# Optimization experiments

Measured on AMD Instinct MI355X. Metric: run time of the kernel, lower is better.

## Reference

```python
import jax, jax.numpy as jnp
import numpy as np

EXPR_NUM = 80
N_PTS = 2_000_000


def setup_inputs() -> dict:
    key = jax.random.key(0)
    ks = jax.random.split(key, 16)
    L, C = 64, 32
    return {
        "expr": jax.random.normal(ks[0], (EXPR_NUM,), jnp.float32) * 0.1,
        "jaw_quat_weight": jax.random.normal(ks[1], (16, 1), jnp.float32) * 0.1,
        "xyz": jax.random.uniform(ks[2], (N_PTS, 3), jnp.float32),
        "feat_lines_x": jax.random.normal(ks[3], (96, L, C), jnp.float32) * 0.02,
        "feat_lines_y": jax.random.normal(ks[4], (96, L, C), jnp.float32) * 0.02,
        "feat_lines_z": jax.random.normal(ks[5], (96, L, C), jnp.float32) * 0.02,
        "w0_v": jax.random.normal(ks[6], (128, 192), jnp.float32) * (1.0 / np.sqrt(192)),
        "w0_g": jax.random.uniform(ks[7], (128,), jnp.float32, 0.5, 1.5),
        "b0": jax.random.normal(ks[8], (128,), jnp.float32) * 0.01,
        "w1_v": jax.random.normal(ks[9], (128, 128), jnp.float32) * (1.0 / np.sqrt(128)),
        "w1_g": jax.random.uniform(ks[10], (128,), jnp.float32, 0.5, 1.5),
        "b1": jax.random.normal(ks[11], (128,), jnp.float32) * 0.01,
        "w2_v": jax.random.normal(ks[12], (1, 128), jnp.float32) * (1.0 / np.sqrt(128)),
        "w2_g": jax.random.uniform(ks[13], (1,), jnp.float32, 0.5, 1.5),
        "b2": jax.random.normal(ks[14], (1,), jnp.float32) * 0.01,
    }


def _wn_linear(x, v, g, b):
    # weight_norm: W = g * v / ||v||_row (norm over input dim)
    norm = jnp.sqrt(jnp.sum(v * v, axis=1))
    W = v * (g / norm)[:, None]
    return x @ W.T + b


def _sample_line(bs_line, jaw_line, pts):
    # bs_line, jaw_line: [L, C]; pts: [N] in [0,1]
    L = bs_line.shape[0]
    p = jnp.clip(pts, 0.0, 1.0) * (L - 1)
    li = jnp.floor(p).astype(jnp.int32)
    ri = jnp.minimum(li + 1, L - 1)
    w = (p - li.astype(p.dtype))[:, None]
    bs = bs_line[li] + w * (bs_line[ri] - bs_line[li])
    jaw = jaw_line[li] + w * (jaw_line[ri] - jaw_line[li])
    return bs, jaw


def reference(expr, jaw_quat_weight, xyz,
              feat_lines_x, feat_lines_y, feat_lines_z,
              w0_v, w0_g, b0, w1_v, w1_g, b1, w2_v, w2_g, b2):
    e = expr.reshape(-1)[:EXPR_NUM]             # [80]
    jw = jaw_quat_weight.reshape(-1)            # [16] (k=1 broadcast in torch einsum)
    # weighted sums over blendshape / jaw pose lines -> [L, C]
    bs_x = jnp.einsum('ilc,i->lc', feat_lines_x[:EXPR_NUM], e)
    bs_y = jnp.einsum('ilc,i->lc', feat_lines_y[:EXPR_NUM], e)
    bs_z = jnp.einsum('ilc,i->lc', feat_lines_z[:EXPR_NUM], e)
    jaw_x = jnp.einsum('ilc,i->lc', feat_lines_x[EXPR_NUM:], jw)
    jaw_y = jnp.einsum('ilc,i->lc', feat_lines_y[EXPR_NUM:], jw)
    jaw_z = jnp.einsum('ilc,i->lc', feat_lines_z[EXPR_NUM:], jw)
    bx, jx = _sample_line(bs_x, jaw_x, xyz[:, 0])
    by, jy = _sample_line(bs_y, jaw_y, xyz[:, 1])
    bz, jz = _sample_line(bs_z, jaw_z, xyz[:, 2])
    fea = jnp.concatenate((bx, by, bz, jx, jy, jz), axis=1)  # [N, 192]
    fea = jax.nn.relu(_wn_linear(fea, w0_v, w0_g, b0))
    fea = jax.nn.relu(_wn_linear(fea, w1_v, w1_g, b1))
    return _wn_linear(fea, w2_v, w2_g, b2)                   # [N, 1]
```

## Files before the change

### kernel.cpp

```cpp
#include <hip/hip_runtime.h>
#include <math.h>

typedef _Float16 h2 __attribute__((ext_vector_type(2)));
typedef _Float16 f16x8 __attribute__((ext_vector_type(8)));
typedef float f32x4 __attribute__((ext_vector_type(4)));


__global__ void precompute_T(const float* __restrict__ expr,
                             const float* __restrict__ jqw,
                             const float* __restrict__ flx,
                             const float* __restrict__ fly,
                             const float* __restrict__ flz,
                             const float* __restrict__ w0v,
                             const float* __restrict__ w0g,
                             const float* __restrict__ b0,
                             float* __restrict__ T) {
    int a = blockIdx.x >> 6;
    int l = blockIdx.x & 63;
    const float* fl = (a == 0) ? flx : (a == 1) ? fly : flz;
    __shared__ float bs[32];
    __shared__ float jaw[32];
    int t = threadIdx.x;
    if (t < 32) {
        float s = 0.f;
        for (int i = 0; i < 80; ++i) s += expr[i] * fl[(i * 64 + l) * 32 + t];
        bs[t] = s;
    } else if (t < 64) {
        int c = t - 32;
        float s = 0.f;
        for (int i = 0; i < 16; ++i) s += jqw[i] * fl[((80 + i) * 64 + l) * 32 + c];
        jaw[c] = s;
    }
    __syncthreads();
    int j = t;
    float ns = 0.f;
    for (int c = 0; c < 192; ++c) { float v = w0v[j * 192 + c]; ns += v * v; }
    float scale = w0g[j] / sqrtf(ns);
    float acc = 0.f;
    for (int c = 0; c < 32; ++c) acc += w0v[j * 192 + a * 32 + c] * bs[c];
    for (int c = 0; c < 32; ++c) acc += w0v[j * 192 + 96 + a * 32 + c] * jaw[c];
    acc *= scale;
    if (a == 0) acc += b0[j];
    T[(a * 64 + l) * 128 + j] = acc;
}

__global__ void precompute_W(const float* __restrict__ w1v,
                             const float* __restrict__ w1g,
                             const float* __restrict__ w2v,
                             const float* __restrict__ w2g,
                             float* __restrict__ W1n,
                             float* __restrict__ w2n) {
    int j = threadIdx.x;
    float ns = 0.f;
    for (int k = 0; k < 128; ++k) { float v = w1v[j * 128 + k]; ns += v * v; }
    float s = w1g[j] / sqrtf(ns);
    for (int k = 0; k < 128; ++k) W1n[j * 128 + k] = w1v[j * 128 + k] * s;
    float n2 = 0.f;
    for (int k = 0; k < 128; ++k) { float v = w2v[k]; n2 += v * v; }
    w2n[j] = w2v[j] * (w2g[0] / sqrtf(n2));
}

#define LDS_T_H2 12288
#define LDS_B_H2 8192

__launch_bounds__(512)
__global__ void mlp_mfma(const float* __restrict__ xyz,
                         const float* __restrict__ Tg,
                         const float* __restrict__ W1g,
                         const float* __restrict__ w2ng,
                         const float* __restrict__ b1,
                         const float* __restrict__ b2p,
                         float* __restrict__ out, int npts) {
    __shared__ __align__(16) h2 tT[LDS_T_H2];
    __shared__ __align__(16) h2 tB[LDS_B_H2];
    int tid = threadIdx.x;

    for (int pi = tid; pi < LDS_T_H2; pi += 512) {
        int r = pi >> 6;
        int p = pi & 63;
        int phys = (r << 6) | (((p >> 2) ^ (r & 15)) << 2) | (p & 3);
        h2 v;
        v.x = (_Float16)Tg[2 * pi];
        v.y = (_Float16)Tg[2 * pi + 1];
        tT[phys] = v;
    }
    for (int pi = tid; pi < LDS_B_H2; pi += 512) {
        int dp = pi & 3;
        int l  = (pi >> 2) & 63;
        int nt = (pi >> 8) & 7;
        int kk = (pi >> 11) & 3;
        int n = nt * 16 + (l & 15);
        int k = kk * 32 + (l >> 4) * 8 + 2 * dp;
        h2 v;
        v.x = (_Float16)W1g[n * 128 + k];
        v.y = (_Float16)W1g[n * 128 + k + 1];
        tB[pi] = v;
    }
    __syncthreads();

    int lane = tid & 63;
    int lp = lane & 15;
    int lg = lane >> 4;
    int waveid = blockIdx.x * 8 + (tid >> 6);
    int nwaves = gridDim.x * 8;
    int ntiles = (npts + 15) >> 4;

    float b1r[8], w2r[8];
#pragma unroll
    for (int nt = 0; nt < 8; ++nt) {
        b1r[nt] = b1[nt * 16 + lp];
        w2r[nt] = w2ng[nt * 16 + lp];
    }
    float b2 = b2p[0];

#pragma unroll 1
    for (int tile = waveid; tile < ntiles; tile += nwaves) {
        int m0 = tile << 4;
        int p = m0 + lp;
        int pc = min(p, npts - 1);
        float cx = xyz[pc * 3 + 0];
        float cy = xyz[pc * 3 + 1];
        float cz = xyz[pc * 3 + 2];

        f16x8 hA[4];
#pragma unroll
        for (int kk = 0; kk < 4; ++kk)
            hA[kk] = (f16x8){0, 0, 0, 0, 0, 0, 0, 0};

#pragma unroll
        for (int a = 0; a < 3; ++a) {
            float v = (a == 0) ? cx : (a == 1) ? cy : cz;
            v = fminf(fmaxf(v, 0.f), 1.f) * 63.f;
            float fv = floorf(v);
            int li = (int)fv;
            int ri = min(li + 1, 63);
            _Float16 w = (_Float16)(v - fv);
            _Float16 wl = (_Float16)1.0f - w;
            f16x8 w8  = {w, w, w, w, w, w, w, w};
            f16x8 wl8 = {wl, wl, wl, wl, wl, wl, wl, wl};
            int rowL = (a * 64 + li) << 4;
            int rowR = (a * 64 + ri) << 4;
            int sl = li & 15;
            int sr = ri & 15;
#pragma unroll
            for (int kk = 0; kk < 4; ++kk) {
                int cidx = lg + 4 * kk;
                f16x8 vl = *reinterpret_cast<const f16x8*>(
                    &tT[(rowL + (cidx ^ sl)) << 2]);
                f16x8 vr = *reinterpret_cast<const f16x8*>(
                    &tT[(rowR + (cidx ^ sr)) << 2]);
                hA[kk] = hA[kk] + vl * wl8 + vr * w8;
            }
        }
        f16x8 z8 = (f16x8){0, 0, 0, 0, 0, 0, 0, 0};
#pragma unroll
        for (int kk = 0; kk < 4; ++kk)
            hA[kk] = __builtin_elementwise_max(hA[kk], z8);

        f32x4 acc[8];
#pragma unroll
        for (int nt = 0; nt < 8; ++nt) acc[nt] = (f32x4){0.f, 0.f, 0.f, 0.f};

#pragma unroll
        for (int kk = 0; kk < 4; ++kk) {
#pragma unroll
            for (int nt = 0; nt < 8; ++nt) {
                f16x8 b = *reinterpret_cast<const f16x8*>(
                    &tB[(((kk * 8 + nt) << 6) | lane) << 2]);
                acc[nt] = __builtin_amdgcn_mfma_f32_16x16x32_f16(
                    hA[kk], b, acc[nt], 0, 0, 0);
            }
        }

        float part0 = 0.f, part1 = 0.f, part2 = 0.f, part3 = 0.f;
#pragma unroll
        for (int nt = 0; nt < 8; ++nt) {
            part0 += w2r[nt] * fmaxf(acc[nt][0] + b1r[nt], 0.f);
            part1 += w2r[nt] * fmaxf(acc[nt][1] + b1r[nt], 0.f);
            part2 += w2r[nt] * fmaxf(acc[nt][2] + b1r[nt], 0.f);
            part3 += w2r[nt] * fmaxf(acc[nt][3] + b1r[nt], 0.f);
        }
#pragma unroll
        for (int mask = 1; mask <= 8; mask <<= 1) {
            part0 += __shfl_xor(part0, mask, 64);
            part1 += __shfl_xor(part1, mask, 64);
            part2 += __shfl_xor(part2, mask, 64);
            part3 += __shfl_xor(part3, mask, 64);
        }
        int mbase = m0 + (lg << 2);
        if (lp == 0 && mbase + 0 < npts) out[mbase + 0] = part0 + b2;
        if (lp == 1 && mbase + 1 < npts) out[mbase + 1] = part1 + b2;
        if (lp == 2 && mbase + 2 < npts) out[mbase + 2] = part2 + b2;
        if (lp == 3 && mbase + 3 < npts) out[mbase + 3] = part3 + b2;
    }
}

extern "C" void kernel_launch(void* const* d_in, const int* in_sizes, int n_in,
                              void* d_out, int out_size, void* d_ws, size_t ws_size,
                              hipStream_t stream) {
    const float* expr = (const float*)d_in[0];
    const float* jqw  = (const float*)d_in[1];
    const float* xyz  = (const float*)d_in[2];
    const float* flx  = (const float*)d_in[3];
    const float* fly  = (const float*)d_in[4];
    const float* flz  = (const float*)d_in[5];
    const float* w0v  = (const float*)d_in[6];
    const float* w0g  = (const float*)d_in[7];
    const float* b0   = (const float*)d_in[8];
    const float* w1v  = (const float*)d_in[9];
    const float* w1g  = (const float*)d_in[10];
    const float* b1   = (const float*)d_in[11];
    const float* w2v  = (const float*)d_in[12];
    const float* w2g  = (const float*)d_in[13];
    const float* b2   = (const float*)d_in[14];

    float* ws = (float*)d_ws;
    float* T   = ws;
    float* W1n = ws + 24576;
    float* w2n = ws + 40960;

    int npts = in_sizes[2] / 3;

    precompute_T<<<192, 128, 0, stream>>>(expr, jqw, flx, fly, flz, w0v, w0g, b0, T);
    precompute_W<<<1, 128, 0, stream>>>(w1v, w1g, w2v, w2g, W1n, w2n);
    mlp_mfma<<<512, 512, 0, stream>>>(xyz, T, W1n, w2n, b1, b2, (float*)d_out, npts);
}
```

Baseline: 254.7 us.

## Keep W1 MFMA B-fragments in registers and reduce with DPP row rotates

Each wave now loads its W1 B-operand fragments once into 32 f16x8 registers instead of staging them in LDS and re-reading them every tile. The 16-lane partial-sum reduction switches from __shfl_xor (ds_bpermute) to DPP row_ror adds, and the kernel is tagged with waves_per_eu(2). This removes LDS traffic and bpermute latency from the inner loop. In exchange it raises VGPR pressure by about 128 registers and lowers occupancy.

```diff
diff --git a/kernel.cpp b/kernel.cpp
--- a/kernel.cpp
+++ b/kernel.cpp
@@ -61,9 +61,16 @@
 }
 
 #define LDS_T_H2 12288
-#define LDS_B_H2 8192
+
+template <int CTRL>
+static __device__ __forceinline__ float dpp_ror_add(float x) {
+    int yi = __builtin_amdgcn_update_dpp(0, __builtin_bit_cast(int, x),
+                                         CTRL, 0xF, 0xF, false);
+    return x + __builtin_bit_cast(float, yi);
+}
 
 __launch_bounds__(512)
+__attribute__((amdgpu_waves_per_eu(2)))
 __global__ void mlp_mfma(const float* __restrict__ xyz,
                          const float* __restrict__ Tg,
                          const float* __restrict__ W1g,
@@ -72,7 +79,6 @@
                          const float* __restrict__ b2p,
                          float* __restrict__ out, int npts) {
     __shared__ __align__(16) h2 tT[LDS_T_H2];
-    __shared__ __align__(16) h2 tB[LDS_B_H2];
     int tid = threadIdx.x;
 
     for (int pi = tid; pi < LDS_T_H2; pi += 512) {
@@ -84,34 +90,36 @@
         v.y = (_Float16)Tg[2 * pi + 1];
         tT[phys] = v;
     }
-    for (int pi = tid; pi < LDS_B_H2; pi += 512) {
-        int dp = pi & 3;
-        int l  = (pi >> 2) & 63;
-        int nt = (pi >> 8) & 7;
-        int kk = (pi >> 11) & 3;
-        int n = nt * 16 + (l & 15);
-        int k = kk * 32 + (l >> 4) * 8 + 2 * dp;
-        h2 v;
-        v.x = (_Float16)W1g[n * 128 + k];
-        v.y = (_Float16)W1g[n * 128 + k + 1];
-        tB[pi] = v;
-    }
     __syncthreads();
 
     int lane = tid & 63;
     int lp = lane & 15;
     int lg = lane >> 4;
+
+    f16x8 Bf[4][8];
+#pragma unroll
+    for (int kk = 0; kk < 4; ++kk) {
+#pragma unroll
+        for (int nt = 0; nt < 8; ++nt) {
+            const float* src = &W1g[(nt * 16 + lp) * 128 + kk * 32 + lg * 8];
+            f16x8 b;
+#pragma unroll
+            for (int j = 0; j < 8; ++j) b[j] = (_Float16)src[j];
+            Bf[kk][nt] = b;
+        }
+    }
+
+    float b1r[8], w2r[8];
+#pragma unroll
+    for (int nt = 0; nt < 8; ++nt) {
+        b1r[nt] = b1[nt * 16 + lp];
+        w2r[nt] = w2ng[nt * 16 + lp];
+    }
+    float b2 = b2p[0];
+
     int waveid = blockIdx.x * 8 + (tid >> 6);
     int nwaves = gridDim.x * 8;
     int ntiles = (npts + 15) >> 4;
-
-    float b1r[8], w2r[8];
-#pragma unroll
-    for (int nt = 0; nt < 8; ++nt) {
-        b1r[nt] = b1[nt * 16 + lp];
-        w2r[nt] = w2ng[nt * 16 + lp];
-    }
-    float b2 = b2p[0];
 
 #pragma unroll 1
     for (int tile = waveid; tile < ntiles; tile += nwaves) {
@@ -165,10 +173,8 @@
         for (int kk = 0; kk < 4; ++kk) {
 #pragma unroll
             for (int nt = 0; nt < 8; ++nt) {
-                f16x8 b = *reinterpret_cast<const f16x8*>(
-                    &tB[(((kk * 8 + nt) << 6) | lane) << 2]);
                 acc[nt] = __builtin_amdgcn_mfma_f32_16x16x32_f16(
-                    hA[kk], b, acc[nt], 0, 0, 0);
+                    hA[kk], Bf[kk][nt], acc[nt], 0, 0, 0);
             }
         }
 
@@ -180,13 +186,23 @@
             part2 += w2r[nt] * fmaxf(acc[nt][2] + b1r[nt], 0.f);
             part3 += w2r[nt] * fmaxf(acc[nt][3] + b1r[nt], 0.f);
         }
-#pragma unroll
-        for (int mask = 1; mask <= 8; mask <<= 1) {
-            part0 += __shfl_xor(part0, mask, 64);
-            part1 += __shfl_xor(part1, mask, 64);
-            part2 += __shfl_xor(part2, mask, 64);
-            part3 += __shfl_xor(part3, mask, 64);
-        }
+        part0 = dpp_ror_add<0x128>(part0);
+        part1 = dpp_ror_add<0x128>(part1);
+        part2 = dpp_ror_add<0x128>(part2);
+        part3 = dpp_ror_add<0x128>(part3);
+        part0 = dpp_ror_add<0x124>(part0);
+        part1 = dpp_ror_add<0x124>(part1);
+        part2 = dpp_ror_add<0x124>(part2);
+        part3 = dpp_ror_add<0x124>(part3);
+        part0 = dpp_ror_add<0x122>(part0);
+        part1 = dpp_ror_add<0x122>(part1);
+        part2 = dpp_ror_add<0x122>(part2);
+        part3 = dpp_ror_add<0x122>(part3);
+        part0 = dpp_ror_add<0x121>(part0);
+        part1 = dpp_ror_add<0x121>(part1);
+        part2 = dpp_ror_add<0x121>(part2);
+        part3 = dpp_ror_add<0x121>(part3);
+
         int mbase = m0 + (lg << 2);
         if (lp == 0 && mbase + 0 < npts) out[mbase + 0] = part0 + b2;
         if (lp == 1 && mbase + 1 < npts) out[mbase + 1] = part1 + b2;
```

Measured after the change: 272.1 us. +6.8%, slower.
